# Kernel optimization log

Measured on AMD Instinct MI355X. Metric: run time of the kernel, lower is better.

The kernel has to match this reference:

```python
import jax, jax.numpy as jnp
import numpy as np

TOP_K = 2  # num_expert in the torch module


def setup_inputs() -> dict:
    key = jax.random.key(0)
    ks = jax.random.split(key, 8)
    B, C, H, W, E, Dh = 8, 512, 32, 32, 8, 1024
    inputs = jax.random.normal(ks[0], (B, C, H, W), dtype=jnp.float32)
    k = jax.random.uniform(ks[1], (B, 1, 1, 1), dtype=jnp.float32)
    # gate: global-avg-pool + Linear(C -> E)
    Wg = jax.random.normal(ks[2], (C, E), dtype=jnp.float32) / np.sqrt(C)
    bg = jnp.zeros((E,), dtype=jnp.float32)
    # experts: per-expert 2-layer channel MLP (1x1-conv style), modulated by k
    W1 = jax.random.normal(ks[3], (E, C, Dh), dtype=jnp.float32) / np.sqrt(C)
    b1 = jnp.zeros((E, Dh), dtype=jnp.float32)
    W2 = jax.random.normal(ks[4], (E, Dh, C), dtype=jnp.float32) / np.sqrt(Dh)
    b2 = jnp.zeros((E, C), dtype=jnp.float32)
    return {"inputs": inputs, "k": k, "Wg": Wg, "bg": bg,
            "W1": W1, "b1": b1, "W2": W2, "b2": b2}


def reference(inputs, k, Wg, bg, W1, b1, W2, b2):
    B = inputs.shape[0]
    # --- gate: softmax in fp32, cast back (matches F.softmax(dtype=torch.float)) ---
    logits = jnp.mean(inputs, axis=(2, 3)) @ Wg + bg            # [B, E]
    weights = jax.nn.softmax(logits.astype(jnp.float32), axis=1).astype(inputs.dtype)
    topk_w, topk_idx = jax.lax.top_k(weights, TOP_K)            # [B, K]
    # --- scatter top-k gate weights into dense [B, E] mask (training path) ---
    exp_w = jnp.zeros_like(weights).at[jnp.arange(B)[:, None], topk_idx].set(topk_w)
    # --- run ALL experts densely (training-mode math), masked combine ---
    h = jnp.einsum('bchw,ecd->bedhw', inputs, W1) + b1[None, :, :, None, None]
    h = jax.nn.gelu(h, approximate=False)                        # [B,E,Dh,H,W]
    y = jnp.einsum('bedhw,edc->bechw', h, W2) + b2[None, :, :, None, None]
    y = y * k[:, None]                                           # per-sample scalar mod
    out = inputs + jnp.einsum('bechw,be->bchw', y, exp_w)        # residual + weighted sum
    return out
```

## Files before the change

kernel.cpp:

```cpp
#include <hip/hip_runtime.h>
#include <hip/hip_bf16.h>
#include <math.h>


typedef __bf16 bf16_t;
typedef __attribute__((ext_vector_type(8))) __bf16 bf16x8;
typedef __attribute__((ext_vector_type(4))) __bf16 bf16x4;
typedef __attribute__((ext_vector_type(4))) float f32x4;

#define GLDS(g, l) __builtin_amdgcn_global_load_lds(                      \
    (const __attribute__((address_space(1))) void*)(const void*)(g),       \
    (__attribute__((address_space(3))) void*)(void*)(l), 16, 0, 0)

__device__ __forceinline__ float gelu_fast(float x) {
    float z = x * 0.70710678118654752f;
    float az = fabsf(z);
    float t = 1.0f / (1.0f + 0.3275911f * az);
    float p = ((((1.061405429f * t - 1.453152027f) * t + 1.421413741f) * t
                - 0.284496736f) * t + 0.254829592f) * t;
    float e = __expf(-az * az);
    float er = copysignf(1.0f - p * e, z);
    return 0.5f * x * (1.0f + er);
}

__global__ __launch_bounds__(256) void transpose_cvt_all(
    const float* __restrict__ x, const float* __restrict__ W1,
    const float* __restrict__ W2, bf16_t* __restrict__ xT,
    bf16_t* __restrict__ W1t, bf16_t* __restrict__ W2t, float* __restrict__ pp) {
    int id = blockIdx.x;
    const float* src; bf16_t* dst; int Rows, Cols, csh; bool dm = false;
    if (id < 1024)      { src = x;  dst = xT;  Rows = 512;  Cols = 1024; csh = 4; dm = true; }
    else if (id < 2048) { id -= 1024; src = W1; dst = W1t; Rows = 512;  Cols = 1024; csh = 4; }
    else                { id -= 2048; src = W2; dst = W2t; Rows = 1024; Cols = 512; csh = 3; }
    const int bz = id >> 7, t = id & 127;
    const int ct = t & ((1 << csh) - 1), rt = t >> csh;
    const int r0 = rt * 64, c0 = ct * 64;
    __shared__ float tile[64][65];
    const int tid = threadIdx.x;
    const int lrw = tid >> 4, lcol = (tid & 15) * 4;
    const float* sb = src + (size_t)bz * Rows * Cols + c0;
    #pragma unroll
    for (int p = 0; p < 4; ++p) {
        const int row = p * 16 + lrw;
        float4 v = *(const float4*)(sb + (size_t)(r0 + row) * Cols + lcol);
        tile[row][lcol + 0] = v.x; tile[row][lcol + 1] = v.y;
        tile[row][lcol + 2] = v.z; tile[row][lcol + 3] = v.w;
    }
    __syncthreads();
    if (dm) {
        const int row = tid >> 2, q = tid & 3;
        float s = 0.f;
        #pragma unroll
        for (int j = 0; j < 16; ++j) s += tile[row][q * 16 + j];
        s += __shfl_down(s, 2, 4);
        s += __shfl_down(s, 1, 4);
        if (q == 0) pp[(bz * 16 + ct) * 512 + r0 + row] = s;
    }
    bf16_t* db = dst + (size_t)bz * Rows * Cols + r0;
    #pragma unroll
    for (int q = 0; q < 2; ++q) {
        const int idq = q * 256 + tid;
        const int orow = idq >> 3, seg = idq & 7;
        bf16_t ov[8];
        #pragma unroll
        for (int j = 0; j < 8; ++j) ov[j] = (bf16_t)tile[seg * 8 + j][orow];
        *(bf16x8*)(db + (size_t)(c0 + orow) * Rows + seg * 8) = *(bf16x8*)ov;
    }
}

__global__ void gate_kernel(const float* __restrict__ pp, const float* __restrict__ Wg,
                            const float* __restrict__ bg, const float* __restrict__ kmod,
                            int* __restrict__ tidx, float* __restrict__ scale) {
    const int tid = threadIdx.x;
    const int b = tid >> 6, l = tid & 63;
    float a[8] = {0.f, 0.f, 0.f, 0.f, 0.f, 0.f, 0.f, 0.f};
    for (int c = l; c < 512; c += 64) {
        float m = 0.f;
        #pragma unroll
        for (int ht = 0; ht < 16; ++ht) m += pp[(b * 16 + ht) * 512 + c];
        #pragma unroll
        for (int e = 0; e < 8; ++e) a[e] += m * Wg[c * 8 + e];
    }
    #pragma unroll
    for (int e = 0; e < 8; ++e)
        #pragma unroll
        for (int off = 32; off; off >>= 1) a[e] += __shfl_xor(a[e], off, 64);
    if (l == 0) {
        float lg[8], mx = -1e30f;
        #pragma unroll
        for (int e = 0; e < 8; ++e) { lg[e] = a[e] * (1.0f / 1024.0f) + bg[e]; mx = fmaxf(mx, lg[e]); }
        float sum = 0.f;
        #pragma unroll
        for (int e = 0; e < 8; ++e) { lg[e] = expf(lg[e] - mx); sum += lg[e]; }
        float inv = 1.0f / sum;
        float best = -1.f; int i0 = 0;
        for (int j = 0; j < 8; ++j) { float w = lg[j] * inv; if (w > best) { best = w; i0 = j; } }
        float best2 = -1.f; int i1 = 0;
        for (int j = 0; j < 8; ++j) { if (j == i0) continue; float w = lg[j] * inv; if (w > best2) { best2 = w; i1 = j; } }
        float kb = kmod[b];
        tidx[b * 2] = i0; tidx[b * 2 + 1] = i1;
        scale[b * 2] = best * kb; scale[b * 2 + 1] = best2 * kb;
    }
}

__global__ __launch_bounds__(256, 4) void gemm1_kernel(
    const bf16_t* __restrict__ W1t, const bf16_t* __restrict__ xT,
    const float* __restrict__ b1, const int* __restrict__ tidx,
    const float* __restrict__ scale, bf16_t* __restrict__ hT) {
    __shared__ bf16_t smem[16384];
    const int bid = blockIdx.x;
    const int pair = bid >> 6, rem = bid & 63;
    const int b = pair >> 1, slot = pair & 1;
    const int e = tidx[pair];
    const float s = scale[pair];
    const int d0 = (rem >> 3) * 128, n0 = (rem & 7) * 128;
    const int tid = threadIdx.x;
    const int lane = tid & 63, wave = tid >> 6;
    const int wm = (wave & 1) * 64, wn = (wave >> 1) * 64;
    const int lrow = lane & 15, quad = lane >> 4;

    const bf16_t* gA = W1t + (size_t)e * 524288 + (size_t)d0 * 512;
    const bf16_t* gB = xT + (size_t)b * 524288 + (size_t)n0 * 512;
    const int r0s = tid >> 2, kcs = (tid & 3) * 8;

    f32x4 acc[4][4];
    #pragma unroll
    for (int i = 0; i < 4; ++i)
        #pragma unroll
        for (int j = 0; j < 4; ++j) acc[i][j] = (f32x4){0.f, 0.f, 0.f, 0.f};

    GLDS(gA + r0s * 512 + kcs, smem + tid * 8);
    GLDS(gA + (64 + r0s) * 512 + kcs, smem + (256 + tid) * 8);
    GLDS(gB + r0s * 512 + kcs, smem + 8192 + tid * 8);
    GLDS(gB + (64 + r0s) * 512 + kcs, smem + 8192 + (256 + tid) * 8);
    __syncthreads();

    for (int it = 0; it < 16; ++it) {
        const int cur = it & 1;
        if (it < 15) {
            const int kn = (it + 1) * 32;
            bf16_t* dA = smem + (cur ^ 1) * 4096;
            bf16_t* dB = smem + 8192 + (cur ^ 1) * 4096;
            GLDS(gA + r0s * 512 + kn + kcs, dA + tid * 8);
            GLDS(gA + (64 + r0s) * 512 + kn + kcs, dA + (256 + tid) * 8);
            GLDS(gB + r0s * 512 + kn + kcs, dB + tid * 8);
            GLDS(gB + (64 + r0s) * 512 + kn + kcs, dB + (256 + tid) * 8);
        }
        const bf16_t* cA = smem + cur * 4096;
        const bf16_t* cB = smem + 8192 + cur * 4096;
        bf16x8 af[4], bfr[4];
        #pragma unroll
        for (int i = 0; i < 4; ++i) {
            af[i] = *(const bf16x8*)&cA[(wm + i * 16 + lrow) * 32 + quad * 8];
            bfr[i] = *(const bf16x8*)&cB[(wn + i * 16 + lrow) * 32 + quad * 8];
        }
        #pragma unroll
        for (int i = 0; i < 4; ++i)
            #pragma unroll
            for (int j = 0; j < 4; ++j)
                acc[i][j] = __builtin_amdgcn_mfma_f32_16x16x32_bf16(af[i], bfr[j], acc[i][j], 0, 0, 0);
        __syncthreads();
    }

    bf16_t* hTb = hT + (size_t)b * 2097152 + slot * 1024;
    float4 bb[4];
    #pragma unroll
    for (int i = 0; i < 4; ++i)
        bb[i] = *(const float4*)(b1 + e * 1024 + d0 + wm + i * 16 + quad * 4);

    #pragma unroll
    for (int half = 0; half < 2; ++half) {
        if (wn == half * 64) {
            #pragma unroll
            for (int i = 0; i < 4; ++i)
                #pragma unroll
                for (int j = 0; j < 4; ++j) {
                    const int hw_l = j * 16 + lrow;
                    const int d_l = wm + i * 16 + quad * 4;
                    f32x4 a = acc[i][j];
                    bf16x4 o = { (bf16_t)(gelu_fast(a[0] + bb[i].x) * s),
                                 (bf16_t)(gelu_fast(a[1] + bb[i].y) * s),
                                 (bf16_t)(gelu_fast(a[2] + bb[i].z) * s),
                                 (bf16_t)(gelu_fast(a[3] + bb[i].w) * s) };
                    *(bf16x4*)&smem[hw_l * 136 + d_l] = o;
                }
        }
        __syncthreads();
        #pragma unroll
        for (int q = 0; q < 4; ++q) {
            const int cid = q * 256 + tid;
            const int row = cid >> 4, c16 = cid & 15;
            bf16x8 v = *(const bf16x8*)&smem[row * 136 + c16 * 8];
            *(bf16x8*)(hTb + (size_t)(n0 + half * 64 + row) * 2048 + d0 + c16 * 8) = v;
        }
        __syncthreads();
    }
}

__global__ __launch_bounds__(256, 5) void gemm2_kernel(
    const bf16_t* __restrict__ W2t, const bf16_t* __restrict__ hT,
    const float* __restrict__ b2, const int* __restrict__ tidx,
    const float* __restrict__ scale, const float* __restrict__ x,
    float* __restrict__ out) {
    __shared__ bf16_t smem[16384];
    const int bid = blockIdx.x;
    const int b = bid >> 7, rem = bid & 127;
    const int c0 = (rem >> 4) * 64, n0 = (rem & 15) * 64;
    const int e0 = tidx[b * 2], e1 = tidx[b * 2 + 1];
    const float s0 = scale[b * 2], s1 = scale[b * 2 + 1];
    const int tid = threadIdx.x;
    const int lane = tid & 63, wave = tid >> 6;
    const int wm = (wave & 1) * 32, wn = (wave >> 1) * 32;
    const int lrow = lane & 15, quad = lane >> 4;

    const bf16_t* hTb = hT + (size_t)b * 2097152 + (size_t)n0 * 2048;
    const bf16_t* A0 = W2t + (size_t)e0 * 524288 + (size_t)c0 * 1024;
    const bf16_t* A1 = W2t + (size_t)e1 * 524288 + (size_t)c0 * 1024;
    const int sr = tid >> 2, kcs = (tid & 3) * 8;

    f32x4 acc[2][2];
    #pragma unroll
    for (int i = 0; i < 2; ++i)
        #pragma unroll
        for (int j = 0; j < 2; ++j) acc[i][j] = (f32x4){0.f, 0.f, 0.f, 0.f};

    auto stage = [&](int st, int it) {
        const int k0 = it * 64;
        const bf16_t* gA = ((k0 < 1024) ? A0 : A1) + (size_t)sr * 1024 + (k0 & 1023);
        bf16_t* dA = smem + st * 4096;
        bf16_t* dB = smem + 8192 + st * 4096;
        GLDS(gA + kcs, dA + tid * 8);
        GLDS(gA + 32 + kcs, dA + 2048 + tid * 8);
        const bf16_t* gBp = hTb + (size_t)sr * 2048 + k0;
        GLDS(gBp + kcs, dB + tid * 8);
        GLDS(gBp + 32 + kcs, dB + 2048 + tid * 8);
    };

    stage(0, 0);
    __syncthreads();

    for (int it = 0; it < 32; ++it) {
        const int cur = it & 1;
        if (it < 31) stage(cur ^ 1, it + 1);
        const bf16_t* cA = smem + cur * 4096;
        const bf16_t* cB = smem + 8192 + cur * 4096;
        #pragma unroll
        for (int ks = 0; ks < 2; ++ks) {
            bf16x8 af[2], bfr[2];
            #pragma unroll
            for (int i = 0; i < 2; ++i) {
                af[i] = *(const bf16x8*)&cA[ks * 2048 + (wm + i * 16 + lrow) * 32 + quad * 8];
                bfr[i] = *(const bf16x8*)&cB[ks * 2048 + (wn + i * 16 + lrow) * 32 + quad * 8];
            }
            #pragma unroll
            for (int i = 0; i < 2; ++i)
                #pragma unroll
                for (int j = 0; j < 2; ++j)
                    acc[i][j] = __builtin_amdgcn_mfma_f32_16x16x32_bf16(af[i], bfr[j], acc[i][j], 0, 0, 0);
        }
        __syncthreads();
    }

    #pragma unroll
    for (int i = 0; i < 2; ++i) {
        const int c_l = c0 + wm + i * 16 + quad * 4;
        const float4 bA = *(const float4*)(b2 + e0 * 512 + c_l);
        const float4 bB = *(const float4*)(b2 + e1 * 512 + c_l);
        const float bias[4] = { s0 * bA.x + s1 * bB.x, s0 * bA.y + s1 * bB.y,
                                s0 * bA.z + s1 * bB.z, s0 * bA.w + s1 * bB.w };
        #pragma unroll
        for (int j = 0; j < 2; ++j) {
            const int hw = n0 + wn + j * 16 + lrow;
            #pragma unroll
            for (int r = 0; r < 4; ++r) {
                const size_t o = (size_t)(b * 512 + c_l + r) * 1024 + hw;
                out[o] = x[o] + acc[i][j][r] + bias[r];
            }
        }
    }
}

extern "C" void kernel_launch(void* const* d_in, const int* in_sizes, int n_in,
                              void* d_out, int out_size, void* d_ws, size_t ws_size,
                              hipStream_t stream) {
    const float* x    = (const float*)d_in[0];
    const float* kmod = (const float*)d_in[1];
    const float* Wg   = (const float*)d_in[2];
    const float* bg   = (const float*)d_in[3];
    const float* W1   = (const float*)d_in[4];
    const float* b1   = (const float*)d_in[5];
    const float* W2   = (const float*)d_in[6];
    const float* b2   = (const float*)d_in[7];
    float* out = (float*)d_out;

    char* ws = (char*)d_ws;
    int*   tix  = (int*)ws;
    float* scl  = (float*)(ws + 64);
    bf16_t* xT  = (bf16_t*)(ws + 32768);
    bf16_t* W1t = (bf16_t*)(ws + 32768 + (size_t)8388608);
    bf16_t* W2t = (bf16_t*)(ws + 32768 + (size_t)2 * 8388608);
    bf16_t* hT  = (bf16_t*)(ws + 32768 + (size_t)3 * 8388608);
    float* pp   = (float*)hT;

    transpose_cvt_all<<<3072, 256, 0, stream>>>(x, W1, W2, xT, W1t, W2t, pp);
    gate_kernel<<<1, 512, 0, stream>>>(pp, Wg, bg, kmod, tix, scl);
    gemm1_kernel<<<1024, 256, 0, stream>>>(W1t, xT, b1, tix, scl, hT);
    gemm2_kernel<<<1024, 256, 0, stream>>>(W2t, hT, b2, tix, scl, x, out);
}
```

Measured before the change: 179.8 us.

## Restructure both expert GEMMs with swizzled K=64 LDS tiles and larger gemm2 tiles

gemm1 moves from double-buffered K=32 steps to single-buffered K=64 steps with an XOR-swizzled LDS layout meant to avoid bank conflicts. It also writes the whole 128x128 epilogue tile in one pass. gemm2 swaps operand roles so hw is the M dimension, uses 128x64 tiles with swizzled K=64 double buffering, and halves the grid. Its epilogue now does vectorised float4 residual loads and stores. gemm1 loses its load/compute overlap and gemm2 runs at lower occupancy, which may hurt latency hiding.

```diff
diff --git a/kernel.cpp b/kernel.cpp
--- a/kernel.cpp
+++ b/kernel.cpp
@@ -107,7 +107,7 @@
     const bf16_t* __restrict__ W1t, const bf16_t* __restrict__ xT,
     const float* __restrict__ b1, const int* __restrict__ tidx,
     const float* __restrict__ scale, bf16_t* __restrict__ hT) {
-    __shared__ bf16_t smem[16384];
+    __shared__ bf16_t smem[17408];
     const int bid = blockIdx.x;
     const int pair = bid >> 6, rem = bid & 63;
     const int b = pair >> 1, slot = pair & 1;
@@ -121,7 +121,6 @@
 
     const bf16_t* gA = W1t + (size_t)e * 524288 + (size_t)d0 * 512;
     const bf16_t* gB = xT + (size_t)b * 524288 + (size_t)n0 * 512;
-    const int r0s = tid >> 2, kcs = (tid & 3) * 8;
 
     f32x4 acc[4][4];
     #pragma unroll
@@ -129,111 +128,103 @@
         #pragma unroll
         for (int j = 0; j < 4; ++j) acc[i][j] = (f32x4){0.f, 0.f, 0.f, 0.f};
 
-    GLDS(gA + r0s * 512 + kcs, smem + tid * 8);
-    GLDS(gA + (64 + r0s) * 512 + kcs, smem + (256 + tid) * 8);
-    GLDS(gB + r0s * 512 + kcs, smem + 8192 + tid * 8);
-    GLDS(gB + (64 + r0s) * 512 + kcs, smem + 8192 + (256 + tid) * 8);
-    __syncthreads();
-
-    for (int it = 0; it < 16; ++it) {
-        const int cur = it & 1;
-        if (it < 15) {
-            const int kn = (it + 1) * 32;
-            bf16_t* dA = smem + (cur ^ 1) * 4096;
-            bf16_t* dB = smem + 8192 + (cur ^ 1) * 4096;
-            GLDS(gA + r0s * 512 + kn + kcs, dA + tid * 8);
-            GLDS(gA + (64 + r0s) * 512 + kn + kcs, dA + (256 + tid) * 8);
-            GLDS(gB + r0s * 512 + kn + kcs, dB + tid * 8);
-            GLDS(gB + (64 + r0s) * 512 + kn + kcs, dB + (256 + tid) * 8);
-        }
-        const bf16_t* cA = smem + cur * 4096;
-        const bf16_t* cB = smem + 8192 + cur * 4096;
-        bf16x8 af[4], bfr[4];
-        #pragma unroll
-        for (int i = 0; i < 4; ++i) {
-            af[i] = *(const bf16x8*)&cA[(wm + i * 16 + lrow) * 32 + quad * 8];
-            bfr[i] = *(const bf16x8*)&cB[(wn + i * 16 + lrow) * 32 + quad * 8];
-        }
-        #pragma unroll
-        for (int i = 0; i < 4; ++i)
-            #pragma unroll
-            for (int j = 0; j < 4; ++j)
-                acc[i][j] = __builtin_amdgcn_mfma_f32_16x16x32_bf16(af[i], bfr[j], acc[i][j], 0, 0, 0);
+    for (int it = 0; it < 8; ++it) {
+        const int k0 = it * 64;
+        #pragma unroll
+        for (int p = 0; p < 4; ++p) {
+            const int row = p * 32 + (tid >> 3);
+            const int cg = ((tid & 7) ^ (row & 7)) * 8;
+            GLDS(gA + (size_t)row * 512 + k0 + cg, smem + (p * 256 + tid) * 8);
+            GLDS(gB + (size_t)row * 512 + k0 + cg, smem + 8192 + (p * 256 + tid) * 8);
+        }
         __syncthreads();
-    }
-
-    bf16_t* hTb = hT + (size_t)b * 2097152 + slot * 1024;
-    float4 bb[4];
-    #pragma unroll
-    for (int i = 0; i < 4; ++i)
-        bb[i] = *(const float4*)(b1 + e * 1024 + d0 + wm + i * 16 + quad * 4);
-
-    #pragma unroll
-    for (int half = 0; half < 2; ++half) {
-        if (wn == half * 64) {
+        #pragma unroll
+        for (int kh = 0; kh < 2; ++kh) {
+            const int swz = ((kh * 4 + quad) ^ (lrow & 7)) * 8;
+            bf16x8 af[4], bfr[4];
+            #pragma unroll
+            for (int i = 0; i < 4; ++i) {
+                af[i]  = *(const bf16x8*)&smem[(wm + i * 16 + lrow) * 64 + swz];
+                bfr[i] = *(const bf16x8*)&smem[8192 + (wn + i * 16 + lrow) * 64 + swz];
+            }
             #pragma unroll
             for (int i = 0; i < 4; ++i)
                 #pragma unroll
-                for (int j = 0; j < 4; ++j) {
-                    const int hw_l = j * 16 + lrow;
-                    const int d_l = wm + i * 16 + quad * 4;
-                    f32x4 a = acc[i][j];
-                    bf16x4 o = { (bf16_t)(gelu_fast(a[0] + bb[i].x) * s),
-                                 (bf16_t)(gelu_fast(a[1] + bb[i].y) * s),
-                                 (bf16_t)(gelu_fast(a[2] + bb[i].z) * s),
-                                 (bf16_t)(gelu_fast(a[3] + bb[i].w) * s) };
-                    *(bf16x4*)&smem[hw_l * 136 + d_l] = o;
-                }
+                for (int j = 0; j < 4; ++j)
+                    acc[i][j] = __builtin_amdgcn_mfma_f32_16x16x32_bf16(af[i], bfr[j], acc[i][j], 0, 0, 0);
         }
         __syncthreads();
-        #pragma unroll
-        for (int q = 0; q < 4; ++q) {
-            const int cid = q * 256 + tid;
-            const int row = cid >> 4, c16 = cid & 15;
-            bf16x8 v = *(const bf16x8*)&smem[row * 136 + c16 * 8];
-            *(bf16x8*)(hTb + (size_t)(n0 + half * 64 + row) * 2048 + d0 + c16 * 8) = v;
-        }
-        __syncthreads();
-    }
-}
-
-__global__ __launch_bounds__(256, 5) void gemm2_kernel(
+    }
+
+    bf16_t* hTb = hT + (size_t)b * 2097152 + slot * 1024;
+    #pragma unroll
+    for (int i = 0; i < 4; ++i) {
+        const int d_l = wm + i * 16 + quad * 4;
+        const float4 bb = *(const float4*)(b1 + e * 1024 + d0 + d_l);
+        #pragma unroll
+        for (int j = 0; j < 4; ++j) {
+            const int hw_l = wn + j * 16 + lrow;
+            f32x4 a = acc[i][j];
+            bf16x4 o = { (bf16_t)(gelu_fast(a[0] + bb.x) * s),
+                         (bf16_t)(gelu_fast(a[1] + bb.y) * s),
+                         (bf16_t)(gelu_fast(a[2] + bb.z) * s),
+                         (bf16_t)(gelu_fast(a[3] + bb.w) * s) };
+            *(bf16x4*)&smem[hw_l * 136 + d_l] = o;
+        }
+    }
+    __syncthreads();
+    #pragma unroll
+    for (int q = 0; q < 8; ++q) {
+        const int idx = q * 256 + tid;
+        const int row = idx >> 4, c16 = idx & 15;
+        bf16x8 v = *(const bf16x8*)&smem[row * 136 + c16 * 8];
+        *(bf16x8*)(hTb + (size_t)(n0 + row) * 2048 + d0 + c16 * 8) = v;
+    }
+}
+
+__global__ __launch_bounds__(256, 2) void gemm2_kernel(
     const bf16_t* __restrict__ W2t, const bf16_t* __restrict__ hT,
     const float* __restrict__ b2, const int* __restrict__ tidx,
     const float* __restrict__ scale, const float* __restrict__ x,
     float* __restrict__ out) {
-    __shared__ bf16_t smem[16384];
+    __shared__ bf16_t smem[24576];
     const int bid = blockIdx.x;
-    const int b = bid >> 7, rem = bid & 127;
-    const int c0 = (rem >> 4) * 64, n0 = (rem & 15) * 64;
+    const int b = bid >> 6, rem = bid & 63;
+    const int c0 = (rem >> 3) * 64, hw0 = (rem & 7) * 128;
     const int e0 = tidx[b * 2], e1 = tidx[b * 2 + 1];
     const float s0 = scale[b * 2], s1 = scale[b * 2 + 1];
     const int tid = threadIdx.x;
     const int lane = tid & 63, wave = tid >> 6;
-    const int wm = (wave & 1) * 32, wn = (wave >> 1) * 32;
+    const int wm = (wave & 1) * 64;
+    const int wc = (wave >> 1) * 32;
     const int lrow = lane & 15, quad = lane >> 4;
 
-    const bf16_t* hTb = hT + (size_t)b * 2097152 + (size_t)n0 * 2048;
-    const bf16_t* A0 = W2t + (size_t)e0 * 524288 + (size_t)c0 * 1024;
-    const bf16_t* A1 = W2t + (size_t)e1 * 524288 + (size_t)c0 * 1024;
-    const int sr = tid >> 2, kcs = (tid & 3) * 8;
-
-    f32x4 acc[2][2];
-    #pragma unroll
-    for (int i = 0; i < 2; ++i)
+    const bf16_t* hTb = hT + (size_t)b * 2097152 + (size_t)hw0 * 2048;
+    const bf16_t* B0 = W2t + (size_t)e0 * 524288 + (size_t)c0 * 1024;
+    const bf16_t* B1 = W2t + (size_t)e1 * 524288 + (size_t)c0 * 1024;
+
+    f32x4 acc[4][2];
+    #pragma unroll
+    for (int i = 0; i < 4; ++i)
         #pragma unroll
         for (int j = 0; j < 2; ++j) acc[i][j] = (f32x4){0.f, 0.f, 0.f, 0.f};
 
     auto stage = [&](int st, int it) {
         const int k0 = it * 64;
-        const bf16_t* gA = ((k0 < 1024) ? A0 : A1) + (size_t)sr * 1024 + (k0 & 1023);
-        bf16_t* dA = smem + st * 4096;
-        bf16_t* dB = smem + 8192 + st * 4096;
-        GLDS(gA + kcs, dA + tid * 8);
-        GLDS(gA + 32 + kcs, dA + 2048 + tid * 8);
-        const bf16_t* gBp = hTb + (size_t)sr * 2048 + k0;
-        GLDS(gBp + kcs, dB + tid * 8);
-        GLDS(gBp + 32 + kcs, dB + 2048 + tid * 8);
+        bf16_t* dst = smem + st * 12288;
+        #pragma unroll
+        for (int p = 0; p < 4; ++p) {
+            const int row = p * 32 + (tid >> 3);
+            const int cg = ((tid & 7) ^ (row & 7)) * 8;
+            GLDS(hTb + (size_t)row * 2048 + k0 + cg, dst + (p * 256 + tid) * 8);
+        }
+        const bf16_t* gB = ((it < 16) ? B0 : B1) + (k0 & 1023);
+        #pragma unroll
+        for (int p = 0; p < 2; ++p) {
+            const int row = p * 32 + (tid >> 3);
+            const int cg = ((tid & 7) ^ (row & 7)) * 8;
+            GLDS(gB + (size_t)row * 1024 + cg, dst + 8192 + (p * 256 + tid) * 8);
+        }
     };
 
     stage(0, 0);
@@ -242,18 +233,20 @@
     for (int it = 0; it < 32; ++it) {
         const int cur = it & 1;
         if (it < 31) stage(cur ^ 1, it + 1);
-        const bf16_t* cA = smem + cur * 4096;
-        const bf16_t* cB = smem + 8192 + cur * 4096;
-        #pragma unroll
-        for (int ks = 0; ks < 2; ++ks) {
-            bf16x8 af[2], bfr[2];
-            #pragma unroll
-            for (int i = 0; i < 2; ++i) {
-                af[i] = *(const bf16x8*)&cA[ks * 2048 + (wm + i * 16 + lrow) * 32 + quad * 8];
-                bfr[i] = *(const bf16x8*)&cB[ks * 2048 + (wn + i * 16 + lrow) * 32 + quad * 8];
-            }
-            #pragma unroll
-            for (int i = 0; i < 2; ++i)
+        const bf16_t* cA = smem + cur * 12288;
+        const bf16_t* cB = cA + 8192;
+        #pragma unroll
+        for (int kh = 0; kh < 2; ++kh) {
+            const int swz = ((kh * 4 + quad) ^ (lrow & 7)) * 8;
+            bf16x8 af[4], bfr[2];
+            #pragma unroll
+            for (int i = 0; i < 4; ++i)
+                af[i] = *(const bf16x8*)&cA[(wm + i * 16 + lrow) * 64 + swz];
+            #pragma unroll
+            for (int j = 0; j < 2; ++j)
+                bfr[j] = *(const bf16x8*)&cB[(wc + j * 16 + lrow) * 64 + swz];
+            #pragma unroll
+            for (int i = 0; i < 4; ++i)
                 #pragma unroll
                 for (int j = 0; j < 2; ++j)
                     acc[i][j] = __builtin_amdgcn_mfma_f32_16x16x32_bf16(af[i], bfr[j], acc[i][j], 0, 0, 0);
@@ -262,20 +255,17 @@
     }
 
     #pragma unroll
-    for (int i = 0; i < 2; ++i) {
-        const int c_l = c0 + wm + i * 16 + quad * 4;
-        const float4 bA = *(const float4*)(b2 + e0 * 512 + c_l);
-        const float4 bB = *(const float4*)(b2 + e1 * 512 + c_l);
-        const float bias[4] = { s0 * bA.x + s1 * bB.x, s0 * bA.y + s1 * bB.y,
-                                s0 * bA.z + s1 * bB.z, s0 * bA.w + s1 * bB.w };
-        #pragma unroll
-        for (int j = 0; j < 2; ++j) {
-            const int hw = n0 + wn + j * 16 + lrow;
-            #pragma unroll
-            for (int r = 0; r < 4; ++r) {
-                const size_t o = (size_t)(b * 512 + c_l + r) * 1024 + hw;
-                out[o] = x[o] + acc[i][j][r] + bias[r];
-            }
+    for (int j = 0; j < 2; ++j) {
+        const int c = c0 + wc + j * 16 + lrow;
+        const float bias = s0 * b2[e0 * 512 + c] + s1 * b2[e1 * 512 + c];
+        #pragma unroll
+        for (int i = 0; i < 4; ++i) {
+            const int hw = hw0 + wm + i * 16 + quad * 4;
+            const size_t o = ((size_t)(b * 512 + c)) * 1024 + hw;
+            const float4 xv = *(const float4*)(x + o);
+            float4 ov = { acc[i][j][0] + xv.x + bias, acc[i][j][1] + xv.y + bias,
+                          acc[i][j][2] + xv.z + bias, acc[i][j][3] + xv.w + bias };
+            *(float4*)(out + o) = ov;
         }
     }
 }
@@ -305,5 +295,5 @@
     transpose_cvt_all<<<3072, 256, 0, stream>>>(x, W1, W2, xT, W1t, W2t, pp);
     gate_kernel<<<1, 512, 0, stream>>>(pp, Wg, bg, kmod, tix, scl);
     gemm1_kernel<<<1024, 256, 0, stream>>>(W1t, xT, b1, tix, scl, hT);
-    gemm2_kernel<<<1024, 256, 0, stream>>>(W2t, hT, b2, tix, scl, x, out);
-}
+    gemm2_kernel<<<512, 256, 0, stream>>>(W2t, hT, b2, tix, scl, x, out);
+}
```

Result: faster. 174.9 us (-2.7%).
